# Kernel optimization log

Hardware: AMD Instinct MI355X
Metric: run time of the kernel (lower is better)

Reference implementation:

```python
import jax, jax.numpy as jnp
import numpy as np

IN, H = 40, 64

def setup_inputs() -> dict:
    key = jax.random.key(0)
    ks = jax.random.split(key, 10)
    s_ih = 1.0 / np.sqrt(H)
    return {
        "x": jax.random.normal(ks[0], (1024, 500, IN), dtype=jnp.float32),
        "W_ih": jax.random.uniform(ks[1], (4 * H, IN), minval=-s_ih, maxval=s_ih, dtype=jnp.float32),
        "W_hh": jax.random.uniform(ks[2], (4 * H, H), minval=-s_ih, maxval=s_ih, dtype=jnp.float32),
        "b_ih": jax.random.uniform(ks[3], (4 * H,), minval=-s_ih, maxval=s_ih, dtype=jnp.float32),
        "b_hh": jax.random.uniform(ks[4], (4 * H,), minval=-s_ih, maxval=s_ih, dtype=jnp.float32),
        "fc1_w": jax.random.uniform(ks[5], (H, H), minval=-s_ih, maxval=s_ih, dtype=jnp.float32),
        "fc1_b": jax.random.uniform(ks[6], (H,), minval=-s_ih, maxval=s_ih, dtype=jnp.float32),
        "fc2_w": jax.random.uniform(ks[7], (2, H), minval=-s_ih, maxval=s_ih, dtype=jnp.float32),
        "fc2_b": jax.random.uniform(ks[8], (2,), minval=-s_ih, maxval=s_ih, dtype=jnp.float32),
    }

def _lstm_last_hidden(x, W_ih, W_hh, b_ih, b_hh):
    B = x.shape[0]
    # Precompute input projections for all timesteps in one big GEMM: [B,T,4H]
    x_proj = jnp.einsum('bti,gi->btg', x, W_ih) + (b_ih + b_hh)
    x_proj_t = jnp.swapaxes(x_proj, 0, 1)  # [T,B,4H] for scan over time

    def step(carry, xp):
        h, c = carry
        z = xp + h @ W_hh.T  # [B,4H], PyTorch gate order: i,f,g,o
        i = jax.nn.sigmoid(z[:, 0 * H:1 * H])
        f = jax.nn.sigmoid(z[:, 1 * H:2 * H])
        g = jnp.tanh(z[:, 2 * H:3 * H])
        o = jax.nn.sigmoid(z[:, 3 * H:4 * H])
        c = f * c + i * g
        h = o * jnp.tanh(c)
        return (h, c), None

    h0 = jnp.zeros((B, H), dtype=x.dtype)
    (h_last, _), _ = jax.lax.scan(step, (h0, h0), x_proj_t)
    return h_last  # [B,H]

def reference(x, W_ih, W_hh, b_ih, b_hh, fc1_w, fc1_b, fc2_w, fc2_b):
    h = _lstm_last_hidden(x, W_ih, W_hh, b_ih, b_hh)
    h = jax.nn.relu(h @ fc1_w.T + fc1_b)
    return h @ fc2_w.T + fc2_b  # [B,2]
```

## Files before the change

kernel.cpp:

```cpp
#include <hip/hip_runtime.h>

#define IN_DIM 40
#define HID 64
#define TSTEPS 500
#define NCH 2
#define ROWB 192
#define SLABP (NCH * ROWB)

typedef _Float16 half8 __attribute__((ext_vector_type(8)));
typedef float    f32x4 __attribute__((ext_vector_type(4)));

#define L2E  1.4426950408889634f
#define L2E2 2.8853900817779268f

__device__ __forceinline__ float exp2_fast(float x) {
    return __builtin_amdgcn_exp2f(x);
}

__device__ __forceinline__ void block_sync_lds() {
    asm volatile("s_waitcnt lgkmcnt(0)" ::: "memory");
    __builtin_amdgcn_s_barrier();
    asm volatile("" ::: "memory");
}

__global__ __launch_bounds__(256, 2)
void lstm_mfma(const float* __restrict__ x,
               const float* __restrict__ W_ih,
               const float* __restrict__ W_hh,
               const float* __restrict__ b_ih,
               const float* __restrict__ b_hh,
               const float* __restrict__ fc1_w,
               const float* __restrict__ fc1_b,
               const float* __restrict__ fc2_w,
               const float* __restrict__ fc2_b,
               float* __restrict__ out)
{
    const int tid = threadIdx.x;
    const int w   = tid >> 6;
    const int l   = tid & 63;
    const int lr  = l & 15;
    const int lg  = l >> 4;
    const int ch  = lr & 1;
    const int jj  = lr >> 1;
    const bool own = (lr < 8);
    const int blk = blockIdx.x;

    __shared__ __align__(16) unsigned char slab[2 * SLABP];
    __shared__ float h32[NCH][HID];
    __shared__ float rl [NCH][HID];

    if (tid < SLABP / 16) reinterpret_cast<uint4*>(slab)[tid] = uint4{0, 0, 0, 0};

    half8 wfrag[4][4];
    f32x4 biasr[4];
    #pragma unroll
    for (int j = 0; j < 4; ++j) {
        const int jt   = 4 * w + j;
        const int unit = 4 * jt + (lr >> 2);
        const int gate = lr & 3;
        const int row  = gate * HID + unit;
        const float sc = (gate == 2) ? L2E2 : L2E;
        #pragma unroll
        for (int kt = 0; kt < 4; ++kt) {
            const int k0 = kt * 32 + lg * 8;
            float v[8];
            if (k0 < 64) {
                const float4* p = reinterpret_cast<const float4*>(W_hh + (size_t)row * HID + k0);
                float4 q0 = p[0], q1 = p[1];
                v[0]=q0.x; v[1]=q0.y; v[2]=q0.z; v[3]=q0.w;
                v[4]=q1.x; v[5]=q1.y; v[6]=q1.z; v[7]=q1.w;
            } else if (k0 < 104) {
                const float4* p = reinterpret_cast<const float4*>(W_ih + (size_t)row * IN_DIM + (k0 - 64));
                float4 q0 = p[0], q1 = p[1];
                v[0]=q0.x; v[1]=q0.y; v[2]=q0.z; v[3]=q0.w;
                v[4]=q1.x; v[5]=q1.y; v[6]=q1.z; v[7]=q1.w;
            } else {
                #pragma unroll
                for (int e = 0; e < 8; ++e) v[e] = 0.0f;
            }
            half8 hv;
            #pragma unroll
            for (int e = 0; e < 8; ++e) hv[e] = (_Float16)(v[e] * sc);
            wfrag[j][kt] = hv;
        }
        const int ud = 4 * jt + lg;
        biasr[j] = f32x4{ (b_ih[0 * HID + ud] + b_hh[0 * HID + ud]) * L2E,
                          (b_ih[1 * HID + ud] + b_hh[1 * HID + ud]) * L2E,
                          (b_ih[2 * HID + ud] + b_hh[2 * HID + ud]) * L2E2,
                          (b_ih[3 * HID + ud] + b_hh[3 * HID + ud]) * L2E };
    }

    const float* xrow = x + ((size_t)(blk * NCH + ch) * TSTEPS) * IN_DIM;
    const float* xg2  = xrow + lg * 8;
    const float* xg3  = xrow + 32;

    f32x4 xaccA[4], xaccB[4];
    {
        float4 p0 = *reinterpret_cast<const float4*>(xg2);
        float4 p1 = *reinterpret_cast<const float4*>(xg2 + 4);
        float4 p2 = *reinterpret_cast<const float4*>(xg3);
        float4 p3 = *reinterpret_cast<const float4*>(xg3 + 4);
        half8 xf2 = { (_Float16)p0.x, (_Float16)p0.y, (_Float16)p0.z, (_Float16)p0.w,
                      (_Float16)p1.x, (_Float16)p1.y, (_Float16)p1.z, (_Float16)p1.w };
        half8 xf3 = { (_Float16)p2.x, (_Float16)p2.y, (_Float16)p2.z, (_Float16)p2.w,
                      (_Float16)p3.x, (_Float16)p3.y, (_Float16)p3.z, (_Float16)p3.w };
        #pragma unroll
        for (int j = 0; j < 4; ++j) {
            f32x4 a = biasr[j];
            a = __builtin_amdgcn_mfma_f32_16x16x32_f16(wfrag[j][2], xf2, a, 0, 0, 0);
            a = __builtin_amdgcn_mfma_f32_16x16x32_f16(wfrag[j][3], xf3, a, 0, 0, 0);
            xaccA[j] = a;
        }
    }
    float4 rA0 = *reinterpret_cast<const float4*>(xg2 + IN_DIM);
    float4 rA1 = *reinterpret_cast<const float4*>(xg2 + IN_DIM + 4);
    float4 rA2 = *reinterpret_cast<const float4*>(xg3 + IN_DIM);
    float4 rA3 = *reinterpret_cast<const float4*>(xg3 + IN_DIM + 4);
    float4 rB0, rB1, rB2, rB3;

    __syncthreads();

    float cs = 0.0f;
    const int uown = 16 * w + 4 * (jj & 3) + lg;

    auto step = [&](int t, int par, f32x4 (&xacc)[4], f32x4 (&xnxt)[4],
                    const float4& c0, const float4& c1, const float4& c2, const float4& c3,
                    float4& n0, float4& n1, float4& n2, float4& n3) {
        const bool lastt = (t == TSTEPS - 1);
        const unsigned char* sb = slab + par * SLABP + ch * ROWB;
        uint4 q0 = *reinterpret_cast<const uint4*>(sb + lg * 16);
        uint4 q1 = *reinterpret_cast<const uint4*>(sb + 64 + lg * 16);
        {
            const size_t toff = (size_t)((t + 2 < TSTEPS) ? t + 2 : TSTEPS - 1) * IN_DIM;
            n0 = *reinterpret_cast<const float4*>(xg2 + toff);
            n1 = *reinterpret_cast<const float4*>(xg2 + toff + 4);
            n2 = *reinterpret_cast<const float4*>(xg3 + toff);
            n3 = *reinterpret_cast<const float4*>(xg3 + toff + 4);
        }
        __builtin_amdgcn_s_setprio(1);
        half8 bf0 = __builtin_bit_cast(half8, q0);
        half8 bf1 = __builtin_bit_cast(half8, q1);
        f32x4 acc[4];
        #pragma unroll
        for (int j = 0; j < 4; ++j) {
            f32x4 a = xacc[j];
            a = __builtin_amdgcn_mfma_f32_16x16x32_f16(wfrag[j][0], bf0, a, 0, 0, 0);
            a = __builtin_amdgcn_mfma_f32_16x16x32_f16(wfrag[j][1], bf1, a, 0, 0, 0);
            acc[j] = a;
        }
        float z0, z1, z2, z3;
        {
            float t01, t23;
            t01 = (jj & 1) ? acc[1][0] : acc[0][0];
            t23 = (jj & 1) ? acc[3][0] : acc[2][0];
            z0  = (jj & 2) ? t23 : t01;
            t01 = (jj & 1) ? acc[1][1] : acc[0][1];
            t23 = (jj & 1) ? acc[3][1] : acc[2][1];
            z1  = (jj & 2) ? t23 : t01;
            t01 = (jj & 1) ? acc[1][2] : acc[0][2];
            t23 = (jj & 1) ? acc[3][2] : acc[2][2];
            z2  = (jj & 2) ? t23 : t01;
            t01 = (jj & 1) ? acc[1][3] : acc[0][3];
            t23 = (jj & 1) ? acc[3][3] : acc[2][3];
            z3  = (jj & 2) ? t23 : t01;
        }
        float iv = __builtin_amdgcn_rcpf(1.0f + exp2_fast(-z0));
        float fv = __builtin_amdgcn_rcpf(1.0f + exp2_fast(-z1));
        float ov = __builtin_amdgcn_rcpf(1.0f + exp2_fast(-z3));
        float e2 = exp2_fast(-fabsf(z2));
        float gv = copysignf((1.0f - e2) * __builtin_amdgcn_rcpf(1.0f + e2), z2);
        cs = fmaf(fv, cs, iv * gv);
        float ec = exp2_fast(-fabsf(cs * L2E2));
        float h  = ov * copysignf((1.0f - ec) * __builtin_amdgcn_rcpf(1.0f + ec), cs);
        if (lastt) {
            if (own) h32[ch][uown] = h;
        } else if (own) {
            unsigned char* db = slab + (par ^ 1) * SLABP + ch * ROWB + uown * 2;
            _Float16 hf = (_Float16)h;
            *reinterpret_cast<unsigned short*>(db) = __builtin_bit_cast(unsigned short, hf);
        }
        __builtin_amdgcn_s_setprio(0);
        {
            half8 xf2 = { (_Float16)c0.x, (_Float16)c0.y, (_Float16)c0.z, (_Float16)c0.w,
                          (_Float16)c1.x, (_Float16)c1.y, (_Float16)c1.z, (_Float16)c1.w };
            half8 xf3 = { (_Float16)c2.x, (_Float16)c2.y, (_Float16)c2.z, (_Float16)c2.w,
                          (_Float16)c3.x, (_Float16)c3.y, (_Float16)c3.z, (_Float16)c3.w };
            #pragma unroll
            for (int j = 0; j < 4; ++j) {
                f32x4 a = biasr[j];
                a = __builtin_amdgcn_mfma_f32_16x16x32_f16(wfrag[j][2], xf2, a, 0, 0, 0);
                a = __builtin_amdgcn_mfma_f32_16x16x32_f16(wfrag[j][3], xf3, a, 0, 0, 0);
                xnxt[j] = a;
            }
        }
        block_sync_lds();
    };

    #pragma unroll 1
    for (int t = 0; t < TSTEPS; t += 2) {
        step(t,     0, xaccA, xaccB, rA0, rA1, rA2, rA3, rB0, rB1, rB2, rB3);
        step(t + 1, 1, xaccB, xaccA, rB0, rB1, rB2, rB3, rA0, rA1, rA2, rA3);
    }

    if (w < NCH) {
        float acc = fc1_b[l];
        const float4* fwp = reinterpret_cast<const float4*>(fc1_w + (size_t)l * HID);
        #pragma unroll
        for (int q = 0; q < 16; ++q) {
            float4 wv = fwp[q];
            float4 hv = reinterpret_cast<const float4*>(&h32[w][0])[q];
            acc = fmaf(wv.x, hv.x, acc);
            acc = fmaf(wv.y, hv.y, acc);
            acc = fmaf(wv.z, hv.z, acc);
            acc = fmaf(wv.w, hv.w, acc);
        }
        rl[w][l] = fmaxf(acc, 0.0f);
    }
    __syncthreads();
    if (tid < NCH * 2) {
        const int c = tid >> 1;
        const int o = tid & 1;
        float acc = fc2_b[o];
        for (int k = 0; k < HID; ++k)
            acc = fmaf(fc2_w[o * HID + k], rl[c][k], acc);
        out[(size_t)(blk * NCH + c) * 2 + o] = acc;
    }
}

extern "C" void kernel_launch(void* const* d_in, const int* in_sizes, int n_in,
                              void* d_out, int out_size, void* d_ws, size_t ws_size,
                              hipStream_t stream) {
    const float* x     = (const float*)d_in[0];
    const float* W_ih  = (const float*)d_in[1];
    const float* W_hh  = (const float*)d_in[2];
    const float* b_ih  = (const float*)d_in[3];
    const float* b_hh  = (const float*)d_in[4];
    const float* fc1_w = (const float*)d_in[5];
    const float* fc1_b = (const float*)d_in[6];
    const float* fc2_w = (const float*)d_in[7];
    const float* fc2_b = (const float*)d_in[8];
    float* out = (float*)d_out;

    const int B = in_sizes[0] / (TSTEPS * IN_DIM);
    lstm_mfma<<<B / NCH, 256, 0, stream>>>(x, W_ih, W_hh, b_ih, b_hh,
                                           fc1_w, fc1_b, fc2_w, fc2_b, out);
}
```

Before: 254.2 us.

## Halve block to two waves with eight gate tiles per wave

Shrinks each block from four waves to two, so every wave holds eight weight tiles and every lane owns one hidden unit. The goal is cheaper per-step barriers and less idle lane work. The input-projection MFMAs now run inside each step on the critical path instead of being pipelined one step ahead, and the bias is added after selection. It drops the s_setprio hints and shortens the x prefetch distance to one step. Two-wave blocks reduce occupancy and latency hiding, and with 8x4 weight fragments per wave register pressure may rise.

```diff
diff --git a/kernel.cpp b/kernel.cpp
--- a/kernel.cpp
+++ b/kernel.cpp
@@ -23,7 +23,7 @@
     asm volatile("" ::: "memory");
 }
 
-__global__ __launch_bounds__(256, 2)
+__global__ __launch_bounds__(128, 1)
 void lstm_mfma(const float* __restrict__ x,
                const float* __restrict__ W_ih,
                const float* __restrict__ W_hh,
@@ -42,7 +42,6 @@
     const int lg  = l >> 4;
     const int ch  = lr & 1;
     const int jj  = lr >> 1;
-    const bool own = (lr < 8);
     const int blk = blockIdx.x;
 
     __shared__ __align__(16) unsigned char slab[2 * SLABP];
@@ -51,11 +50,10 @@
 
     if (tid < SLABP / 16) reinterpret_cast<uint4*>(slab)[tid] = uint4{0, 0, 0, 0};
 
-    half8 wfrag[4][4];
-    f32x4 biasr[4];
+    half8 wfrag[8][4];
     #pragma unroll
-    for (int j = 0; j < 4; ++j) {
-        const int jt   = 4 * w + j;
+    for (int j = 0; j < 8; ++j) {
+        const int jt   = 8 * w + j;
         const int unit = 4 * jt + (lr >> 2);
         const int gate = lr & 3;
         const int row  = gate * HID + unit;
@@ -83,87 +81,72 @@
             for (int e = 0; e < 8; ++e) hv[e] = (_Float16)(v[e] * sc);
             wfrag[j][kt] = hv;
         }
-        const int ud = 4 * jt + lg;
-        biasr[j] = f32x4{ (b_ih[0 * HID + ud] + b_hh[0 * HID + ud]) * L2E,
-                          (b_ih[1 * HID + ud] + b_hh[1 * HID + ud]) * L2E,
-                          (b_ih[2 * HID + ud] + b_hh[2 * HID + ud]) * L2E2,
-                          (b_ih[3 * HID + ud] + b_hh[3 * HID + ud]) * L2E };
-    }
+    }
+
+    const int uown = 32 * w + 4 * jj + lg;
+    const f32x4 biasown = {
+        (b_ih[0 * HID + uown] + b_hh[0 * HID + uown]) * L2E,
+        (b_ih[1 * HID + uown] + b_hh[1 * HID + uown]) * L2E,
+        (b_ih[2 * HID + uown] + b_hh[2 * HID + uown]) * L2E2,
+        (b_ih[3 * HID + uown] + b_hh[3 * HID + uown]) * L2E };
 
     const float* xrow = x + ((size_t)(blk * NCH + ch) * TSTEPS) * IN_DIM;
     const float* xg2  = xrow + lg * 8;
     const float* xg3  = xrow + 32;
 
-    f32x4 xaccA[4], xaccB[4];
-    {
-        float4 p0 = *reinterpret_cast<const float4*>(xg2);
-        float4 p1 = *reinterpret_cast<const float4*>(xg2 + 4);
-        float4 p2 = *reinterpret_cast<const float4*>(xg3);
-        float4 p3 = *reinterpret_cast<const float4*>(xg3 + 4);
-        half8 xf2 = { (_Float16)p0.x, (_Float16)p0.y, (_Float16)p0.z, (_Float16)p0.w,
-                      (_Float16)p1.x, (_Float16)p1.y, (_Float16)p1.z, (_Float16)p1.w };
-        half8 xf3 = { (_Float16)p2.x, (_Float16)p2.y, (_Float16)p2.z, (_Float16)p2.w,
-                      (_Float16)p3.x, (_Float16)p3.y, (_Float16)p3.z, (_Float16)p3.w };
-        #pragma unroll
-        for (int j = 0; j < 4; ++j) {
-            f32x4 a = biasr[j];
-            a = __builtin_amdgcn_mfma_f32_16x16x32_f16(wfrag[j][2], xf2, a, 0, 0, 0);
-            a = __builtin_amdgcn_mfma_f32_16x16x32_f16(wfrag[j][3], xf3, a, 0, 0, 0);
-            xaccA[j] = a;
-        }
-    }
-    float4 rA0 = *reinterpret_cast<const float4*>(xg2 + IN_DIM);
-    float4 rA1 = *reinterpret_cast<const float4*>(xg2 + IN_DIM + 4);
-    float4 rA2 = *reinterpret_cast<const float4*>(xg3 + IN_DIM);
-    float4 rA3 = *reinterpret_cast<const float4*>(xg3 + IN_DIM + 4);
-    float4 rB0, rB1, rB2, rB3;
+    float4 xb0 = *reinterpret_cast<const float4*>(xg2);
+    float4 xb1 = *reinterpret_cast<const float4*>(xg2 + 4);
+    float4 xb2 = *reinterpret_cast<const float4*>(xg3);
+    float4 xb3 = *reinterpret_cast<const float4*>(xg3 + 4);
 
     __syncthreads();
 
     float cs = 0.0f;
-    const int uown = 16 * w + 4 * (jj & 3) + lg;
-
-    auto step = [&](int t, int par, f32x4 (&xacc)[4], f32x4 (&xnxt)[4],
-                    const float4& c0, const float4& c1, const float4& c2, const float4& c3,
-                    float4& n0, float4& n1, float4& n2, float4& n3) {
-        const bool lastt = (t == TSTEPS - 1);
+
+    auto step = [&](int t, int par, bool lastt) {
         const unsigned char* sb = slab + par * SLABP + ch * ROWB;
         uint4 q0 = *reinterpret_cast<const uint4*>(sb + lg * 16);
         uint4 q1 = *reinterpret_cast<const uint4*>(sb + 64 + lg * 16);
+        half8 xf2 = { (_Float16)xb0.x, (_Float16)xb0.y, (_Float16)xb0.z, (_Float16)xb0.w,
+                      (_Float16)xb1.x, (_Float16)xb1.y, (_Float16)xb1.z, (_Float16)xb1.w };
+        half8 xf3 = { (_Float16)xb2.x, (_Float16)xb2.y, (_Float16)xb2.z, (_Float16)xb2.w,
+                      (_Float16)xb3.x, (_Float16)xb3.y, (_Float16)xb3.z, (_Float16)xb3.w };
+        f32x4 xacc[8];
+        #pragma unroll
+        for (int j = 0; j < 8; ++j) {
+            f32x4 a = f32x4{0.0f, 0.0f, 0.0f, 0.0f};
+            a = __builtin_amdgcn_mfma_f32_16x16x32_f16(wfrag[j][2], xf2, a, 0, 0, 0);
+            a = __builtin_amdgcn_mfma_f32_16x16x32_f16(wfrag[j][3], xf3, a, 0, 0, 0);
+            xacc[j] = a;
+        }
         {
-            const size_t toff = (size_t)((t + 2 < TSTEPS) ? t + 2 : TSTEPS - 1) * IN_DIM;
-            n0 = *reinterpret_cast<const float4*>(xg2 + toff);
-            n1 = *reinterpret_cast<const float4*>(xg2 + toff + 4);
-            n2 = *reinterpret_cast<const float4*>(xg3 + toff);
-            n3 = *reinterpret_cast<const float4*>(xg3 + toff + 4);
-        }
-        __builtin_amdgcn_s_setprio(1);
+            const size_t toff = (size_t)((t + 1 < TSTEPS) ? t + 1 : TSTEPS - 1) * IN_DIM;
+            xb0 = *reinterpret_cast<const float4*>(xg2 + toff);
+            xb1 = *reinterpret_cast<const float4*>(xg2 + toff + 4);
+            xb2 = *reinterpret_cast<const float4*>(xg3 + toff);
+            xb3 = *reinterpret_cast<const float4*>(xg3 + toff + 4);
+        }
         half8 bf0 = __builtin_bit_cast(half8, q0);
         half8 bf1 = __builtin_bit_cast(half8, q1);
-        f32x4 acc[4];
-        #pragma unroll
-        for (int j = 0; j < 4; ++j) {
-            f32x4 a = xacc[j];
-            a = __builtin_amdgcn_mfma_f32_16x16x32_f16(wfrag[j][0], bf0, a, 0, 0, 0);
+        f32x4 zs;
+        #pragma unroll
+        for (int j = 0; j < 8; ++j) {
+            f32x4 a = __builtin_amdgcn_mfma_f32_16x16x32_f16(wfrag[j][0], bf0, xacc[j], 0, 0, 0);
             a = __builtin_amdgcn_mfma_f32_16x16x32_f16(wfrag[j][1], bf1, a, 0, 0, 0);
-            acc[j] = a;
-        }
-        float z0, z1, z2, z3;
-        {
-            float t01, t23;
-            t01 = (jj & 1) ? acc[1][0] : acc[0][0];
-            t23 = (jj & 1) ? acc[3][0] : acc[2][0];
-            z0  = (jj & 2) ? t23 : t01;
-            t01 = (jj & 1) ? acc[1][1] : acc[0][1];
-            t23 = (jj & 1) ? acc[3][1] : acc[2][1];
-            z1  = (jj & 2) ? t23 : t01;
-            t01 = (jj & 1) ? acc[1][2] : acc[0][2];
-            t23 = (jj & 1) ? acc[3][2] : acc[2][2];
-            z2  = (jj & 2) ? t23 : t01;
-            t01 = (jj & 1) ? acc[1][3] : acc[0][3];
-            t23 = (jj & 1) ? acc[3][3] : acc[2][3];
-            z3  = (jj & 2) ? t23 : t01;
-        }
+            if (j == 0) {
+                zs = a;
+            } else {
+                const bool m = (jj == j);
+                zs[0] = m ? a[0] : zs[0];
+                zs[1] = m ? a[1] : zs[1];
+                zs[2] = m ? a[2] : zs[2];
+                zs[3] = m ? a[3] : zs[3];
+            }
+        }
+        float z0 = zs[0] + biasown[0];
+        float z1 = zs[1] + biasown[1];
+        float z2 = zs[2] + biasown[2];
+        float z3 = zs[3] + biasown[3];
         float iv = __builtin_amdgcn_rcpf(1.0f + exp2_fast(-z0));
         float fv = __builtin_amdgcn_rcpf(1.0f + exp2_fast(-z1));
         float ov = __builtin_amdgcn_rcpf(1.0f + exp2_fast(-z3));
@@ -173,36 +156,22 @@
         float ec = exp2_fast(-fabsf(cs * L2E2));
         float h  = ov * copysignf((1.0f - ec) * __builtin_amdgcn_rcpf(1.0f + ec), cs);
         if (lastt) {
-            if (own) h32[ch][uown] = h;
-        } else if (own) {
+            h32[ch][uown] = h;
+        } else {
             unsigned char* db = slab + (par ^ 1) * SLABP + ch * ROWB + uown * 2;
             _Float16 hf = (_Float16)h;
             *reinterpret_cast<unsigned short*>(db) = __builtin_bit_cast(unsigned short, hf);
         }
-        __builtin_amdgcn_s_setprio(0);
-        {
-            half8 xf2 = { (_Float16)c0.x, (_Float16)c0.y, (_Float16)c0.z, (_Float16)c0.w,
-                          (_Float16)c1.x, (_Float16)c1.y, (_Float16)c1.z, (_Float16)c1.w };
-            half8 xf3 = { (_Float16)c2.x, (_Float16)c2.y, (_Float16)c2.z, (_Float16)c2.w,
-                          (_Float16)c3.x, (_Float16)c3.y, (_Float16)c3.z, (_Float16)c3.w };
-            #pragma unroll
-            for (int j = 0; j < 4; ++j) {
-                f32x4 a = biasr[j];
-                a = __builtin_amdgcn_mfma_f32_16x16x32_f16(wfrag[j][2], xf2, a, 0, 0, 0);
-                a = __builtin_amdgcn_mfma_f32_16x16x32_f16(wfrag[j][3], xf3, a, 0, 0, 0);
-                xnxt[j] = a;
-            }
-        }
         block_sync_lds();
     };
 
     #pragma unroll 1
     for (int t = 0; t < TSTEPS; t += 2) {
-        step(t,     0, xaccA, xaccB, rA0, rA1, rA2, rA3, rB0, rB1, rB2, rB3);
-        step(t + 1, 1, xaccB, xaccA, rB0, rB1, rB2, rB3, rA0, rA1, rA2, rA3);
-    }
-
-    if (w < NCH) {
+        step(t,     0, false);
+        step(t + 1, 1, t + 1 == TSTEPS - 1);
+    }
+
+    {
         float acc = fc1_b[l];
         const float4* fwp = reinterpret_cast<const float4*>(fc1_w + (size_t)l * HID);
         #pragma unroll
@@ -242,6 +211,6 @@
     float* out = (float*)d_out;
 
     const int B = in_sizes[0] / (TSTEPS * IN_DIM);
-    lstm_mfma<<<B / NCH, 256, 0, stream>>>(x, W_ih, W_hh, b_ih, b_hh,
+    lstm_mfma<<<B / NCH, 128, 0, stream>>>(x, W_ih, W_hh, b_ih, b_hh,
                                            fc1_w, fc1_b, fc2_w, fc2_b, out);
 }
```

Measured after the change: 336.5 us. +32.4%, slower.
